# Performance work log

Measured on AMD Instinct MI355X. Metric: run time of the kernel, lower is better.

The kernel has to match this reference:

```python
import jax, jax.numpy as jnp
import numpy as np

N_NODES = 100000
N_EDGES = 1600000
IN_F, HID, N_COLORS = 128, 128, 10


def setup_inputs() -> dict:
    key = jax.random.key(0)
    k1, k2, k3, k4 = jax.random.split(key, 4)
    x = jax.random.normal(k1, (N_NODES, IN_F), dtype=jnp.float32)
    edge_index = jax.random.randint(k2, (2, N_EDGES), 0, N_NODES, dtype=jnp.int64)
    # Glorot-ish init for weights
    W1 = jax.random.normal(k3, (IN_F, HID), dtype=jnp.float32) / np.sqrt(IN_F)
    b1 = jnp.zeros((HID,), dtype=jnp.float32)
    W2 = jax.random.normal(k4, (HID, N_COLORS), dtype=jnp.float32) / np.sqrt(HID)
    b2 = jnp.zeros((N_COLORS,), dtype=jnp.float32)
    return {"x": x, "edge_index": edge_index, "W1": W1, "b1": b1, "W2": W2, "b2": b2}


def _gcn_norm(edge_index, num_nodes):
    # Add self-loops, compute symmetric normalization D^-1/2 (A+I) D^-1/2
    loops = jnp.arange(num_nodes, dtype=edge_index.dtype)
    src = jnp.concatenate([edge_index[0], loops])
    dst = jnp.concatenate([edge_index[1], loops])
    deg = jax.ops.segment_sum(jnp.ones_like(dst, dtype=jnp.float32), dst,
                              num_segments=num_nodes)
    deg_isqrt = jax.lax.rsqrt(deg)  # deg >= 1 due to self-loops
    norm = deg_isqrt[src] * deg_isqrt[dst]  # [E + N]
    return src, dst, norm


def _gcn_conv(h, src, dst, norm, num_nodes, W, b):
    # Linear transform first (PyG GCNConv), then gather-scale-scatter aggregate
    h = h @ W                                   # [N, out]
    msg = h[src] * norm[:, None]                # [E + N, out] gather
    out = jax.ops.segment_sum(msg, dst, num_segments=num_nodes)  # scatter-add
    return out + b


def reference(x, edge_index, W1, b1, W2, b2):
    n = x.shape[0]
    src, dst, norm = _gcn_norm(edge_index, n)
    h = _gcn_conv(x, src, dst, norm, n, W1, b1)
    h = jax.nn.relu(h)
    # dropout is identity in eval mode
    h = _gcn_conv(h, src, dst, norm, n, W2, b2)
    return jax.nn.softmax(h, axis=1)
```

## Files before the change

### kernel.cpp

```cpp
#include <hip/hip_runtime.h>
#include <hip/hip_fp16.h>

#define IN_F 128
#define HID  128
#define NC   10
#define H2P  16
#define NPB  128
#define NBMAX 784
#define BCAP 2560
#define CAPP 2944
#define EPB  4096
#define LDW  136

typedef _Float16 f16x8 __attribute__((ext_vector_type(8)));
typedef float f32x4 __attribute__((ext_vector_type(4)));
typedef int int4a __attribute__((ext_vector_type(4), aligned(4)));

__device__ inline __half2 shfl_xor_h2(__half2 v, int mask) {
    int i = __shfl_xor(*reinterpret_cast<int*>(&v), mask, 64);
    return *reinterpret_cast<__half2*>(&i);
}

__global__ __launch_bounds__(1024) void k_bin(const int* __restrict__ src,
                                              const int* __restrict__ dst,
                                              int* __restrict__ bcnt,
                                              unsigned int* __restrict__ binned,
                                              const float* __restrict__ W1,
                                              __half* __restrict__ WT,
                                              const float* __restrict__ W2,
                                              float* __restrict__ W2T,
                                              int E, int nbin) {
    __shared__ int hist[NBMAX];
    __shared__ int base[NBMAX];
    __shared__ int lcur[NBMAX];
    const int tid = threadIdx.x;

    if (blockIdx.x == 0) {
        for (int i = tid; i < IN_F * HID; i += 1024) {
            int k = i >> 7, n = i & 127;
            WT[n * IN_F + k] = __float2half(W1[k * HID + n]);
        }
        for (int i = tid; i < NC * IN_F; i += 1024)
            W2T[i] = W2[(i & 127) * NC + (i >> 7)];
    }

    for (int b = tid; b < nbin; b += 1024) { hist[b] = 0; lcur[b] = 0; }
    __syncthreads();

    const int e0 = blockIdx.x * EPB + tid;
    int d[4];
    #pragma unroll
    for (int u = 0; u < 4; u++) {
        int e = e0 + u * 1024;
        d[u] = (e < E) ? dst[e] : -1;
        if (d[u] >= 0) atomicAdd(&hist[d[u] >> 7], 1);
    }
    __syncthreads();
    for (int b = tid; b < nbin; b += 1024) {
        int h = hist[b];
        base[b] = h ? atomicAdd(&bcnt[b], h) : 0;
    }
    __syncthreads();
    #pragma unroll
    for (int u = 0; u < 4; u++) {
        int e = e0 + u * 1024;
        if (e < E) {
            int dd = d[u];
            int b = dd >> 7;
            int s = src[e];
            int o = base[b] + atomicAdd(&lcur[b], 1);
            if (o < BCAP)
                binned[(size_t)b * BCAP + o] = ((unsigned)(dd & 127) << 17) | (unsigned)s;
        }
    }
}

__global__ __launch_bounds__(256) void k_pg(const int* __restrict__ bcnt,
                                            const unsigned int* __restrict__ binned,
                                            int2* __restrict__ rowinfo,
                                            float* __restrict__ dis,
                                            int* __restrict__ csr,
                                            const float* __restrict__ X,
                                            const __half* __restrict__ WT,
                                            __half* __restrict__ hsh,
                                            __half* __restrict__ h2h,
                                            int N) {
    __shared__ int h[NPB];
    __shared__ int lb[NPB];
    __shared__ int cur[NPB];
    __shared__ float sdis[NPB];
    __shared__ _Float16 sX[32 * LDW];
    __shared__ _Float16 sW[128 * LDW];
    const int b = blockIdx.x;
    const int tid = threadIdx.x;

    if (tid < NPB) h[tid] = 0;
    __syncthreads();

    const int m = min(bcnt[b], BCAP);
    const unsigned int* p = binned + (size_t)b * BCAP;
    for (int i = tid; i < m; i += 256) atomicAdd(&h[p[i] >> 17], 1);
    __syncthreads();

    int myh = 0, cnt4 = 0;
    if (tid < NPB) { myh = h[tid]; cnt4 = (myh + 3) & ~3; lb[tid] = cnt4; }
    __syncthreads();
    #pragma unroll
    for (int off = 1; off < NPB; off <<= 1) {
        int t = (tid < NPB && tid >= off) ? lb[tid - off] : 0;
        __syncthreads();
        if (tid < NPB) lb[tid] += t;
        __syncthreads();
    }
    int ex = 0;
    if (tid < NPB) {
        ex = lb[tid] - cnt4;
        int node = b * NPB + tid;
        if (node < N) {
            rowinfo[node] = make_int2(b * CAPP + ex, cnt4);
            float dd = rsqrtf(1.0f + (float)myh);
            dis[node] = dd;
            sdis[tid] = dd;
        }
        lb[tid] = ex;
        cur[tid] = 0;
    }
    __syncthreads();
    for (int i = tid; i < m; i += 256) {
        unsigned v = p[i];
        int dl = v >> 17;
        int r = atomicAdd(&cur[dl], 1);
        csr[b * CAPP + lb[dl] + r] = (int)(v & 0x1FFFF);
    }
    if (tid < NPB) {
        for (int k = myh; k < cnt4; k++) csr[b * CAPP + ex + k] = N;
    }
    if (b == 0) {
        f16x8 z = {0, 0, 0, 0, 0, 0, 0, 0};
        if (tid < 16) *(f16x8*)(hsh + (size_t)N * HID + tid * 8) = z;
        if (tid < 2)  *(f16x8*)(h2h + (size_t)N * H2P + tid * 8) = z;
    }

    {
        int n = tid >> 1, part = tid & 1;
        const f16x8* srcp = (const f16x8*)(WT + n * IN_F + part * 64);
        f16x8* dstp = (f16x8*)(sW + n * LDW + part * 64);
        #pragma unroll
        for (int c = 0; c < 8; c++) dstp[c] = srcp[c];
    }
    const int wave = tid >> 6;
    const int lane = tid & 63;
    const int quad = lane >> 4;
    const int l16 = lane & 15;
    const int nbase = wave * 32;

    for (int tdx = 0; tdx < 4; tdx++) {
        int row0 = b * NPB + tdx * 32;
        if (row0 >= N) break;
        __syncthreads();
        {
            int r = tid >> 3;
            int k0 = (tid & 7) * 16;
            const float* sp = X + (size_t)(row0 + r) * IN_F + k0;
            float4 f0 = *(const float4*)(sp);
            float4 f1 = *(const float4*)(sp + 4);
            float4 f2 = *(const float4*)(sp + 8);
            float4 f3 = *(const float4*)(sp + 12);
            f16x8 h0, h1;
            h0[0] = (_Float16)f0.x; h0[1] = (_Float16)f0.y;
            h0[2] = (_Float16)f0.z; h0[3] = (_Float16)f0.w;
            h0[4] = (_Float16)f1.x; h0[5] = (_Float16)f1.y;
            h0[6] = (_Float16)f1.z; h0[7] = (_Float16)f1.w;
            h1[0] = (_Float16)f2.x; h1[1] = (_Float16)f2.y;
            h1[2] = (_Float16)f2.z; h1[3] = (_Float16)f2.w;
            h1[4] = (_Float16)f3.x; h1[5] = (_Float16)f3.y;
            h1[6] = (_Float16)f3.z; h1[7] = (_Float16)f3.w;
            *(f16x8*)(sX + r * LDW + k0) = h0;
            *(f16x8*)(sX + r * LDW + k0 + 8) = h1;
        }
        __syncthreads();

        f32x4 acc00 = {0,0,0,0}, acc01 = {0,0,0,0}, acc10 = {0,0,0,0}, acc11 = {0,0,0,0};
        #pragma unroll
        for (int kc = 0; kc < 4; kc++) {
            const int koff = kc * 32 + quad * 8;
            f16x8 a0 = *(const f16x8*)(sX + l16 * LDW + koff);
            f16x8 a1 = *(const f16x8*)(sX + (16 + l16) * LDW + koff);
            f16x8 b0 = *(const f16x8*)(sW + (nbase + l16) * LDW + koff);
            f16x8 b1 = *(const f16x8*)(sW + (nbase + 16 + l16) * LDW + koff);
            acc00 = __builtin_amdgcn_mfma_f32_16x16x32_f16(a0, b0, acc00, 0, 0, 0);
            acc01 = __builtin_amdgcn_mfma_f32_16x16x32_f16(a0, b1, acc01, 0, 0, 0);
            acc10 = __builtin_amdgcn_mfma_f32_16x16x32_f16(a1, b0, acc10, 0, 0, 0);
            acc11 = __builtin_amdgcn_mfma_f32_16x16x32_f16(a1, b1, acc11, 0, 0, 0);
        }
        #pragma unroll
        for (int r = 0; r < 4; r++) {
            {
                int lr = tdx * 32 + quad * 4 + r;
                float d = sdis[lr];
                __half* o = hsh + (size_t)(b * NPB + lr) * HID + nbase + l16;
                o[0]  = __float2half(acc00[r] * d);
                o[16] = __float2half(acc01[r] * d);
            }
            {
                int lr = tdx * 32 + 16 + quad * 4 + r;
                float d = sdis[lr];
                __half* o = hsh + (size_t)(b * NPB + lr) * HID + nbase + l16;
                o[0]  = __float2half(acc10[r] * d);
                o[16] = __float2half(acc11[r] * d);
            }
        }
    }
}

__global__ __launch_bounds__(256) void k_agg1(const __half* __restrict__ hsh,
                                              const int2* __restrict__ rowinfo,
                                              const int* __restrict__ csr,
                                              const float* __restrict__ dis,
                                              const float* __restrict__ b1,
                                              const float* __restrict__ W2T,
                                              __half* __restrict__ h2h,
                                              int N) {
    const int node = blockIdx.x * 4 + (threadIdx.x >> 6);
    if (node >= N) return;
    const int lane = threadIdx.x & 63;
    const int g   = lane >> 4;
    const int l16 = lane & 15;
    const int f0  = l16 * 8;
    const __half2 hz = __half2half2(__float2half(0.0f));

    const int2 ri = rowinfo[node];
    const int beg = ri.x, end = ri.x + ri.y;
    const float d = dis[node];

    __half2 acc2[4] = {hz, hz, hz, hz};
    if (g == 0) {
        float4 r = *(const float4*)(hsh + (size_t)node * HID + f0);
        const __half2* hh = (const __half2*)&r;
        acc2[0] = hh[0]; acc2[1] = hh[1]; acc2[2] = hh[2]; acc2[3] = hh[3];
    }

    int j0 = beg + 4 * g;
    if (j0 < end) {
        int4a cv = *(const int4a*)(csr + j0);
        while (true) {
            const int jn = j0 + 16;
            const bool more = (jn < end);
            int4a cvn = cv;
            if (more) cvn = *(const int4a*)(csr + jn);
            float4 r0 = *(const float4*)(hsh + (size_t)cv[0] * HID + f0);
            float4 r1 = *(const float4*)(hsh + (size_t)cv[1] * HID + f0);
            float4 r2 = *(const float4*)(hsh + (size_t)cv[2] * HID + f0);
            float4 r3 = *(const float4*)(hsh + (size_t)cv[3] * HID + f0);
            const __half2* h0 = (const __half2*)&r0;
            const __half2* h1 = (const __half2*)&r1;
            const __half2* h2 = (const __half2*)&r2;
            const __half2* h3 = (const __half2*)&r3;
            #pragma unroll
            for (int i = 0; i < 4; i++) {
                acc2[i] = __hadd2(acc2[i], h0[i]);
                acc2[i] = __hadd2(acc2[i], h1[i]);
                acc2[i] = __hadd2(acc2[i], h2[i]);
                acc2[i] = __hadd2(acc2[i], h3[i]);
            }
            if (!more) break;
            cv = cvn; j0 = jn;
        }
    }

    #pragma unroll
    for (int i = 0; i < 4; i++) {
        acc2[i] = __hadd2(acc2[i], shfl_xor_h2(acc2[i], 16));
        acc2[i] = __hadd2(acc2[i], shfl_xor_h2(acc2[i], 32));
    }
    float acc[8];
    #pragma unroll
    for (int i = 0; i < 4; i++) {
        float2 t = __half22float2(acc2[i]);
        acc[2 * i] = t.x; acc[2 * i + 1] = t.y;
    }

    float4 ba = *(const float4*)(b1 + f0);
    float4 bb = *(const float4*)(b1 + f0 + 4);
    float h[8];
    h[0] = fmaxf(fmaf(d, acc[0], ba.x), 0.0f);
    h[1] = fmaxf(fmaf(d, acc[1], ba.y), 0.0f);
    h[2] = fmaxf(fmaf(d, acc[2], ba.z), 0.0f);
    h[3] = fmaxf(fmaf(d, acc[3], ba.w), 0.0f);
    h[4] = fmaxf(fmaf(d, acc[4], bb.x), 0.0f);
    h[5] = fmaxf(fmaf(d, acc[5], bb.y), 0.0f);
    h[6] = fmaxf(fmaf(d, acc[6], bb.z), 0.0f);
    h[7] = fmaxf(fmaf(d, acc[7], bb.w), 0.0f);

    const int cb = (g == 0) ? 0 : (g == 1) ? 3 : (g == 2) ? 6 : 8;
    const int nc = (g < 2) ? 3 : 2;
    float p[3];
    #pragma unroll
    for (int ci = 0; ci < 3; ci++) {
        if (ci < nc) {
            int c = cb + ci;
            float4 wa = *(const float4*)(W2T + c * IN_F + f0);
            float4 wb = *(const float4*)(W2T + c * IN_F + f0 + 4);
            float t = fmaf(h[0], wa.x, fmaf(h[1], wa.y, fmaf(h[2], wa.z, h[3] * wa.w)));
            t = fmaf(h[4], wb.x, fmaf(h[5], wb.y, fmaf(h[6], wb.z, fmaf(h[7], wb.w, t))));
            #pragma unroll
            for (int off = 1; off < 16; off <<= 1) t += __shfl_xor(t, off, 64);
            p[ci] = t;
        }
    }
    if (l16 == 0) {
        __half* o = h2h + (size_t)node * H2P + cb;
        for (int ci = 0; ci < nc; ci++) o[ci] = __float2half(d * p[ci]);
    }
}

__global__ __launch_bounds__(256) void k_agg2(const __half* __restrict__ h2h,
                                              const int2* __restrict__ rowinfo,
                                              const int* __restrict__ csr,
                                              const float* __restrict__ dis,
                                              const float* __restrict__ b2,
                                              float* __restrict__ out,
                                              int N) {
    int t = blockIdx.x * 256 + threadIdx.x;
    int node = t >> 3;
    if (node >= N) return;
    int o = t & 7;
    int q = o & 1;
    int eg = o >> 1;
    const int base = q * 8;
    const __half2 hz = __half2half2(__float2half(0.0f));

    __half2 a2[4] = {hz, hz, hz, hz};
    if (eg == 0) {
        float4 r = *(const float4*)(h2h + (size_t)node * H2P + base);
        const __half2* hh = (const __half2*)&r;
        a2[0] = hh[0]; a2[1] = hh[1]; a2[2] = hh[2]; a2[3] = hh[3];
    }
    const int2 ri = rowinfo[node];
    const int end = ri.x + ri.y;
    for (int j0 = ri.x + 4 * eg; j0 < end; j0 += 16) {
        int4a cv = *(const int4a*)(csr + j0);
        float4 r0 = *(const float4*)(h2h + (size_t)cv[0] * H2P + base);
        float4 r1 = *(const float4*)(h2h + (size_t)cv[1] * H2P + base);
        float4 r2 = *(const float4*)(h2h + (size_t)cv[2] * H2P + base);
        float4 r3 = *(const float4*)(h2h + (size_t)cv[3] * H2P + base);
        const __half2* h0 = (const __half2*)&r0;
        const __half2* h1 = (const __half2*)&r1;
        const __half2* h2 = (const __half2*)&r2;
        const __half2* h3 = (const __half2*)&r3;
        #pragma unroll
        for (int i = 0; i < 4; i++) {
            a2[i] = __hadd2(a2[i], h0[i]);
            a2[i] = __hadd2(a2[i], h1[i]);
            a2[i] = __hadd2(a2[i], h2[i]);
            a2[i] = __hadd2(a2[i], h3[i]);
        }
    }

    #pragma unroll
    for (int i = 0; i < 4; i++) {
        a2[i] = __hadd2(a2[i], shfl_xor_h2(a2[i], 2));
        a2[i] = __hadd2(a2[i], shfl_xor_h2(a2[i], 4));
    }

    float a[8];
    #pragma unroll
    for (int i = 0; i < 4; i++) {
        float2 tt = __half22float2(a2[i]);
        a[2 * i] = tt.x; a[2 * i + 1] = tt.y;
    }

    const float d = dis[node];
    float vv[8];
    #pragma unroll
    for (int i = 0; i < 8; i++) {
        int f = base + i;
        vv[i] = (f < NC) ? fmaf(d, a[i], b2[f]) : -1e30f;
    }
    float m = vv[0];
    #pragma unroll
    for (int i = 1; i < 8; i++) m = fmaxf(m, vv[i]);
    m = fmaxf(m, __shfl_xor(m, 1, 64));
    float e[8];
    float s = 0.0f;
    #pragma unroll
    for (int i = 0; i < 8; i++) { e[i] = (base + i < NC) ? expf(vv[i] - m) : 0.0f; s += e[i]; }
    s += __shfl_xor(s, 1, 64);
    float inv = 1.0f / s;

    float* op = out + (size_t)node * NC;
    if (o == 0) {
        *(float2*)(op + 0) = make_float2(e[0] * inv, e[1] * inv);
        *(float2*)(op + 2) = make_float2(e[2] * inv, e[3] * inv);
        *(float2*)(op + 4) = make_float2(e[4] * inv, e[5] * inv);
        *(float2*)(op + 6) = make_float2(e[6] * inv, e[7] * inv);
    } else if (o == 1) {
        *(float2*)(op + 8) = make_float2(e[0] * inv, e[1] * inv);
    }
}

extern "C" void kernel_launch(void* const* d_in, const int* in_sizes, int n_in,
                              void* d_out, int out_size, void* d_ws, size_t ws_size,
                              hipStream_t stream) {
    const float* x  = (const float*)d_in[0];
    const int*   ei = (const int*)d_in[1];
    const float* W1 = (const float*)d_in[2];
    const float* b1 = (const float*)d_in[3];
    const float* W2 = (const float*)d_in[4];
    const float* b2 = (const float*)d_in[5];
    float* out = (float*)d_out;

    const int N = in_sizes[0] / IN_F;
    const int E = in_sizes[1] / 2;
    const int* esrc = ei;
    const int* edst = ei + E;
    const int nbin = (N + NPB - 1) / NPB;

    char* ws = (char*)d_ws;
    int2*   rowinfo = (int2*)(ws);
    float*  dis     = (float*)(ws + 0x100000);
    int*    bcnt    = (int*)(ws + 0x180000);
    __half* WT      = (__half*)(ws + 0x190000);
    float*  W2T     = (float*)(ws + 0x1A0000);
    unsigned int* binned = (unsigned int*)(ws + 0x200000);
    int*    csr     = (int*)(ws + 0xA00000);
    __half* hsh     = (__half*)(ws + 0x1400000);
    __half* h2h     = (__half*)(ws + 0x2D00000);

    hipMemsetAsync(bcnt, 0, (size_t)nbin * sizeof(int), stream);

    k_bin <<<(E + EPB - 1) / EPB, 1024, 0, stream>>>(esrc, edst, bcnt, binned, W1, WT, W2, W2T, E, nbin);
    k_pg  <<<nbin, 256, 0, stream>>>(bcnt, binned, rowinfo, dis, csr, x, WT, hsh, h2h, N);
    k_agg1<<<(N + 3) / 4, 256, 0, stream>>>(hsh, rowinfo, csr, dis, b1, W2T, h2h, N);
    k_agg2<<<(int)(((size_t)N * 8 + 255) / 256), 256, 0, stream>>>(h2h, rowinfo, csr, dis, b2, out, N);
}
```

Before: 230.0 us.

## Overlap X@W1 GEMM with edge binning in one merged launch

Adds a combined kernel where the first blocks compute X@W1 with MFMA into an fp32 scratch buffer while the remaining blocks bin edges by destination, so the GEMM and binning run at the same time. A new placement kernel then builds the CSR and degrees and scales and converts the precomputed rows to fp16. In exchange, an fp32 intermediate of N×128 is written and read back. The old path is kept as a fallback when the workspace is too small.

```diff
diff --git a/kernel.cpp b/kernel.cpp
--- a/kernel.cpp
+++ b/kernel.cpp
@@ -19,6 +19,219 @@
 __device__ inline __half2 shfl_xor_h2(__half2 v, int mask) {
     int i = __shfl_xor(*reinterpret_cast<int*>(&v), mask, 64);
     return *reinterpret_cast<__half2*>(&i);
+}
+
+__global__ __launch_bounds__(1024, 4) void k_work(const int* __restrict__ src,
+                                                  const int* __restrict__ dst,
+                                                  int* __restrict__ bcnt,
+                                                  unsigned int* __restrict__ binned,
+                                                  const float* __restrict__ X,
+                                                  const float* __restrict__ W1,
+                                                  const float* __restrict__ W2,
+                                                  float* __restrict__ W2T,
+                                                  float* __restrict__ hraw,
+                                                  int E, int nbin, int N, int NBG) {
+    __shared__ __align__(16) char smem[2 * 128 * LDW * 2 + 512];
+    const int tid = threadIdx.x;
+
+    if (blockIdx.x >= NBG) {
+        int* hist = (int*)smem;
+        int* base = hist + NBMAX;
+        int* lcur = base + NBMAX;
+        for (int b = tid; b < nbin; b += 1024) { hist[b] = 0; lcur[b] = 0; }
+        __syncthreads();
+
+        const int e0 = (blockIdx.x - NBG) * EPB + tid;
+        int d[4];
+        #pragma unroll
+        for (int u = 0; u < 4; u++) {
+            int e = e0 + u * 1024;
+            d[u] = (e < E) ? dst[e] : -1;
+            if (d[u] >= 0) atomicAdd(&hist[d[u] >> 7], 1);
+        }
+        __syncthreads();
+        for (int b = tid; b < nbin; b += 1024) {
+            int h = hist[b];
+            base[b] = h ? atomicAdd(&bcnt[b], h) : 0;
+        }
+        __syncthreads();
+        #pragma unroll
+        for (int u = 0; u < 4; u++) {
+            int e = e0 + u * 1024;
+            if (e < E) {
+                int dd = d[u];
+                int b = dd >> 7;
+                int s = src[e];
+                int o = base[b] + atomicAdd(&lcur[b], 1);
+                if (o < BCAP)
+                    binned[(size_t)b * BCAP + o] = ((unsigned)(dd & 127) << 17) | (unsigned)s;
+            }
+        }
+        return;
+    }
+
+    _Float16* sX = (_Float16*)smem;
+    _Float16* sW = sX + 128 * LDW;
+    const int row0 = blockIdx.x * 128;
+
+    if (blockIdx.x == 0) {
+        for (int i = tid; i < NC * IN_F; i += 1024)
+            W2T[i] = W2[(i & 127) * NC + (i >> 7)];
+    }
+    for (int i = tid; i < IN_F * HID; i += 1024) {
+        int k = i >> 7, n = i & 127;
+        sW[n * LDW + k] = (_Float16)W1[i];
+    }
+    {
+        int r = tid >> 3;
+        int k0 = (tid & 7) * 16;
+        int row = row0 + r; if (row >= N) row = N - 1;
+        const float* sp = X + (size_t)row * IN_F + k0;
+        float4 f0 = *(const float4*)(sp);
+        float4 f1 = *(const float4*)(sp + 4);
+        float4 f2 = *(const float4*)(sp + 8);
+        float4 f3 = *(const float4*)(sp + 12);
+        f16x8 h0, h1;
+        h0[0] = (_Float16)f0.x; h0[1] = (_Float16)f0.y;
+        h0[2] = (_Float16)f0.z; h0[3] = (_Float16)f0.w;
+        h0[4] = (_Float16)f1.x; h0[5] = (_Float16)f1.y;
+        h0[6] = (_Float16)f1.z; h0[7] = (_Float16)f1.w;
+        h1[0] = (_Float16)f2.x; h1[1] = (_Float16)f2.y;
+        h1[2] = (_Float16)f2.z; h1[3] = (_Float16)f2.w;
+        h1[4] = (_Float16)f3.x; h1[5] = (_Float16)f3.y;
+        h1[6] = (_Float16)f3.z; h1[7] = (_Float16)f3.w;
+        *(f16x8*)(sX + r * LDW + k0) = h0;
+        *(f16x8*)(sX + r * LDW + k0 + 8) = h1;
+    }
+    __syncthreads();
+
+    const int wave = tid >> 6;
+    const int sub  = wave >> 2;
+    const int nbase = (wave & 3) * 32;
+    const int lane = tid & 63;
+    const int quad = lane >> 4;
+    const int l16 = lane & 15;
+    const int rbase = sub * 32;
+
+    f32x4 acc00 = {0,0,0,0}, acc01 = {0,0,0,0}, acc10 = {0,0,0,0}, acc11 = {0,0,0,0};
+    #pragma unroll
+    for (int kc = 0; kc < 4; kc++) {
+        const int koff = kc * 32 + quad * 8;
+        f16x8 a0 = *(const f16x8*)(sX + (rbase + l16) * LDW + koff);
+        f16x8 a1 = *(const f16x8*)(sX + (rbase + 16 + l16) * LDW + koff);
+        f16x8 b0 = *(const f16x8*)(sW + (nbase + l16) * LDW + koff);
+        f16x8 b1 = *(const f16x8*)(sW + (nbase + 16 + l16) * LDW + koff);
+        acc00 = __builtin_amdgcn_mfma_f32_16x16x32_f16(a0, b0, acc00, 0, 0, 0);
+        acc01 = __builtin_amdgcn_mfma_f32_16x16x32_f16(a0, b1, acc01, 0, 0, 0);
+        acc10 = __builtin_amdgcn_mfma_f32_16x16x32_f16(a1, b0, acc10, 0, 0, 0);
+        acc11 = __builtin_amdgcn_mfma_f32_16x16x32_f16(a1, b1, acc11, 0, 0, 0);
+    }
+    #pragma unroll
+    for (int r = 0; r < 4; r++) {
+        {
+            int row = row0 + rbase + quad * 4 + r;
+            if (row < N) {
+                float* o = hraw + (size_t)row * HID + nbase + l16;
+                o[0]  = acc00[r];
+                o[16] = acc01[r];
+            }
+        }
+        {
+            int row = row0 + rbase + 16 + quad * 4 + r;
+            if (row < N) {
+                float* o = hraw + (size_t)row * HID + nbase + l16;
+                o[0]  = acc10[r];
+                o[16] = acc11[r];
+            }
+        }
+    }
+}
+
+__global__ __launch_bounds__(256) void k_place(const int* __restrict__ bcnt,
+                                               const unsigned int* __restrict__ binned,
+                                               int2* __restrict__ rowinfo,
+                                               float* __restrict__ dis,
+                                               int* __restrict__ csr,
+                                               const float* __restrict__ hraw,
+                                               __half* __restrict__ hsh,
+                                               __half* __restrict__ h2h,
+                                               int N) {
+    __shared__ int h[NPB];
+    __shared__ int lb[NPB];
+    __shared__ int cur[NPB];
+    __shared__ float sdis[NPB];
+    const int b = blockIdx.x;
+    const int tid = threadIdx.x;
+
+    if (tid < NPB) h[tid] = 0;
+    __syncthreads();
+
+    const int m = min(bcnt[b], BCAP);
+    const unsigned int* p = binned + (size_t)b * BCAP;
+    for (int i = tid; i < m; i += 256) atomicAdd(&h[p[i] >> 17], 1);
+    __syncthreads();
+
+    int myh = 0, cnt4 = 0;
+    if (tid < NPB) { myh = h[tid]; cnt4 = (myh + 3) & ~3; lb[tid] = cnt4; }
+    __syncthreads();
+    #pragma unroll
+    for (int off = 1; off < NPB; off <<= 1) {
+        int t = (tid < NPB && tid >= off) ? lb[tid - off] : 0;
+        __syncthreads();
+        if (tid < NPB) lb[tid] += t;
+        __syncthreads();
+    }
+    int ex = 0;
+    if (tid < NPB) {
+        ex = lb[tid] - cnt4;
+        int node = b * NPB + tid;
+        if (node < N) {
+            rowinfo[node] = make_int2(b * CAPP + ex, cnt4);
+            float dd = rsqrtf(1.0f + (float)myh);
+            dis[node] = dd;
+            sdis[tid] = dd;
+        } else sdis[tid] = 0.0f;
+        lb[tid] = ex;
+        cur[tid] = 0;
+    }
+    __syncthreads();
+    for (int i = tid; i < m; i += 256) {
+        unsigned v = p[i];
+        int dl = v >> 17;
+        int r = atomicAdd(&cur[dl], 1);
+        csr[b * CAPP + lb[dl] + r] = (int)(v & 0x1FFFF);
+    }
+    if (tid < NPB) {
+        for (int k = myh; k < cnt4; k++) csr[b * CAPP + ex + k] = N;
+    }
+    if (b == 0) {
+        f16x8 z = {0, 0, 0, 0, 0, 0, 0, 0};
+        if (tid < 16) *(f16x8*)(hsh + (size_t)N * HID + tid * 8) = z;
+        if (tid < 2)  *(f16x8*)(h2h + (size_t)N * H2P + tid * 8) = z;
+    }
+    __syncthreads();
+
+    {
+        const int r = tid >> 1;
+        const int half = tid & 1;
+        const int node = b * NPB + r;
+        if (node < N) {
+            const float d = sdis[r];
+            const float4* ip = (const float4*)(hraw + (size_t)node * HID + half * 64);
+            __half* op = hsh + (size_t)node * HID + half * 64;
+            #pragma unroll
+            for (int c = 0; c < 8; c++) {
+                float4 fa = ip[2 * c];
+                float4 fb = ip[2 * c + 1];
+                f16x8 hv;
+                hv[0] = (_Float16)(fa.x * d); hv[1] = (_Float16)(fa.y * d);
+                hv[2] = (_Float16)(fa.z * d); hv[3] = (_Float16)(fa.w * d);
+                hv[4] = (_Float16)(fb.x * d); hv[5] = (_Float16)(fb.y * d);
+                hv[6] = (_Float16)(fb.z * d); hv[7] = (_Float16)(fb.w * d);
+                *(f16x8*)(op + c * 8) = hv;
+            }
+        }
+    }
 }
 
 __global__ __launch_bounds__(1024) void k_bin(const int* __restrict__ src,
@@ -415,6 +628,8 @@
     const int* esrc = ei;
     const int* edst = ei + E;
     const int nbin = (N + NPB - 1) / NPB;
+    const int NBG  = (N + 127) / 128;
+    const int NBB  = (E + EPB - 1) / EPB;
 
     char* ws = (char*)d_ws;
     int2*   rowinfo = (int2*)(ws);
@@ -425,12 +640,19 @@
     unsigned int* binned = (unsigned int*)(ws + 0x200000);
     int*    csr     = (int*)(ws + 0xA00000);
     __half* hsh     = (__half*)(ws + 0x1400000);
-    __half* h2h     = (__half*)(ws + 0x2D00000);
+    __half* h2h     = (__half*)(ws + 0x2C80000);
+    float*  hraw    = (float*)(ws + 0x3000000);
 
     hipMemsetAsync(bcnt, 0, (size_t)nbin * sizeof(int), stream);
 
-    k_bin <<<(E + EPB - 1) / EPB, 1024, 0, stream>>>(esrc, edst, bcnt, binned, W1, WT, W2, W2T, E, nbin);
-    k_pg  <<<nbin, 256, 0, stream>>>(bcnt, binned, rowinfo, dis, csr, x, WT, hsh, h2h, N);
+    if (ws_size >= 0x6100000ULL) {
+        k_work <<<NBG + NBB, 1024, 0, stream>>>(esrc, edst, bcnt, binned, x, W1, W2, W2T,
+                                                hraw, E, nbin, N, NBG);
+        k_place<<<nbin, 256, 0, stream>>>(bcnt, binned, rowinfo, dis, csr, hraw, hsh, h2h, N);
+    } else {
+        k_bin <<<NBB, 1024, 0, stream>>>(esrc, edst, bcnt, binned, W1, WT, W2, W2T, E, nbin);
+        k_pg  <<<nbin, 256, 0, stream>>>(bcnt, binned, rowinfo, dis, csr, x, WT, hsh, h2h, N);
+    }
     k_agg1<<<(N + 3) / 4, 256, 0, stream>>>(hsh, rowinfo, csr, dis, b1, W2T, h2h, N);
     k_agg2<<<(int)(((size_t)N * 8 + 255) / 256), 256, 0, stream>>>(h2h, rowinfo, csr, dis, b2, out, N);
 }
```

Measured after the change: 240.8 us. +4.7%, slower.
